# Performance work log

Hardware: AMD Instinct MI355X
Metric: run time of the kernel (lower is better)

Reference implementation:

```python
import jax, jax.numpy as jnp
import numpy as np

B, S, D, H, FF = 2, 2048, 1024, 16, 4096
DK = D // H
LOCAL_WINDOW, STRIDE = 128, 128
NEG = -1000000000.0
EPS = 1e-5


def _layernorm(x, g, b):
    mu = jnp.mean(x, axis=-1, keepdims=True)
    var = jnp.mean(jnp.square(x - mu), axis=-1, keepdims=True)
    return (x - mu) * jax.lax.rsqrt(var + EPS) * g + b


def _strided_mask(seq):
    # allowed(i, j): j <= i and (i-j <= local_window or (i-j) % stride == 0)
    i = jnp.arange(seq)[:, None]
    j = jnp.arange(seq)[None, :]
    d = i - j
    return (d >= 0) & ((d <= LOCAL_WINDOW) | (d % STRIDE == 0))  # [S, S] bool


def setup_inputs() -> dict:
    key = jax.random.key(0)
    ks = jax.random.split(key, 18)
    w = lambda k, shape: jax.random.normal(k, shape, jnp.float32) * 0.02
    return {
        "x": jax.random.normal(ks[0], (B, S, D), jnp.float32),
        "mask": jnp.ones((1, 1, S, S), jnp.int32),
        "Wq": w(ks[1], (D, D)), "bq": jnp.zeros((D,), jnp.float32),
        "Wk": w(ks[2], (D, D)), "bk": jnp.zeros((D,), jnp.float32),
        "Wv": w(ks[3], (D, D)), "bv": jnp.zeros((D,), jnp.float32),
        "Wo": w(ks[4], (D, D)), "bo": jnp.zeros((D,), jnp.float32),
        "W1": w(ks[5], (D, FF)), "bf1": jnp.zeros((FF,), jnp.float32),
        "W2": w(ks[6], (FF, D)), "bf2": jnp.zeros((D,), jnp.float32),
        "g1": jnp.ones((D,), jnp.float32), "bl1": jnp.zeros((D,), jnp.float32),
        "g2": jnp.ones((D,), jnp.float32), "bl2": jnp.zeros((D,), jnp.float32),
    }


def reference(x, mask, Wq, bq, Wk, bk, Wv, bv, Wo, bo,
              W1, bf1, W2, bf2, g1, bl1, g2, bl2):
    b, s, d = x.shape
    sm = _strided_mask(s)[None, None]  # [1,1,S,S]

    # pre-LN self-attention
    n = _layernorm(x, g1, bl1)
    split = lambda t: t.reshape(b, s, H, DK).transpose(0, 2, 1, 3)  # [B,H,S,DK]
    q = split(n @ Wq + bq)
    k = split(n @ Wk + bk)
    v = split(n @ Wv + bv)

    scores = jnp.einsum('bhqd,bhkd->bhqk', q, k) / jnp.sqrt(jnp.float32(DK))
    scores = jnp.where(sm, scores, NEG)          # strided/local mask
    scores = jnp.where(mask == 0, NEG, scores)   # user mask
    attn = jax.nn.softmax(scores, axis=-1)
    o = jnp.einsum('bhqk,bhkd->bhqd', attn, v)
    o = o.transpose(0, 2, 1, 3).reshape(b, s, d) @ Wo + bo
    x = x + o

    # pre-LN FFN (GELU exact, matching torch nn.GELU default)
    n2 = _layernorm(x, g2, bl2)
    ff = jax.nn.gelu(n2 @ W1 + bf1, approximate=False) @ W2 + bf2
    return x + ff
```

## Files before the change

### kernel.cpp

```cpp
#include <hip/hip_runtime.h>
#include <math.h>

typedef unsigned int u32;
typedef unsigned short u16;

#define B_  2
#define S_  2048
#define D_  1024
#define H_  16
#define DK_ 64
#define FF_ 4096
#define NEG_ -1000000000.0f

typedef __attribute__((ext_vector_type(8))) short short8;
typedef __attribute__((ext_vector_type(4))) float floatx4;
typedef __attribute__((ext_vector_type(4))) unsigned short ushort4_t;

__device__ inline u16 f2b(float f) {
    union { float f; u32 u; } v; v.f = f;
    u32 r = (v.u + 0x7fffu + ((v.u >> 16) & 1u)) >> 16;
    return (u16)r;
}
__device__ inline float b2f(u16 b) {
    union { u32 u; float f; } v; v.u = ((u32)b) << 16;
    return v.f;
}

__device__ inline void gl_lds16(const u16* g, u16* l) {
    __builtin_amdgcn_global_load_lds((const __attribute__((address_space(1))) u32*)g,
                                     (__attribute__((address_space(3))) u32*)l, 16, 0, 0);
}

__global__ void tconv4(const float* __restrict__ W0, const float* __restrict__ W1_,
                       const float* __restrict__ W2_, const float* __restrict__ W3,
                       u16* __restrict__ dstBase) {
    __shared__ float tile[32][33];
    int z = blockIdx.z;
    const float* Wm = (z == 0) ? W0 : (z == 1) ? W1_ : (z == 2) ? W2_ : W3;
    u16* Wt = dstBase + (size_t)z * 1024 * 1024;
    const int K = 1024, N = 1024;
    int n0 = blockIdx.x * 32, k0 = blockIdx.y * 32;
    int tx = threadIdx.x & 31, ty = threadIdx.x >> 5;
#pragma unroll
    for (int r = 0; r < 32; r += 8)
        tile[ty + r][tx] = Wm[(size_t)(k0 + ty + r) * N + n0 + tx];
    __syncthreads();
#pragma unroll
    for (int r = 0; r < 32; r += 8)
        Wt[(size_t)(n0 + ty + r) * K + k0 + tx] = f2b(tile[tx][ty + r]);
}

__global__ void tconv(const float* __restrict__ Wm, u16* __restrict__ Wt, int K, int N) {
    __shared__ float tile[32][33];
    int n0 = blockIdx.x * 32, k0 = blockIdx.y * 32;
    int tx = threadIdx.x & 31, ty = threadIdx.x >> 5;
#pragma unroll
    for (int r = 0; r < 32; r += 8)
        tile[ty + r][tx] = Wm[(size_t)(k0 + ty + r) * N + n0 + tx];
    __syncthreads();
#pragma unroll
    for (int r = 0; r < 32; r += 8)
        Wt[(size_t)(n0 + ty + r) * K + k0 + tx] = f2b(tile[tx][ty + r]);
}

__global__ void catbias(const float* __restrict__ bq, const float* __restrict__ bk,
                        const float* __restrict__ bv, float* __restrict__ out) {
    int i = blockIdx.x * 256 + threadIdx.x;
    float v = (i < 1024) ? bq[i] : (i < 2048) ? bk[i - 1024] : bv[i - 2048];
    out[i] = v;
}

__global__ __launch_bounds__(256)
void mask_tiles(const int* __restrict__ mask, int* __restrict__ tflag) {
    int jt = blockIdx.x, it = blockIdx.y;
    const int* base = mask + (size_t)it * 128 * S_ + jt * 128;
    int t = threadIdx.x;
    int ok = 1;
    for (int e = t; e < 128 * 32; e += 256) {
        int r = e >> 5, c4 = e & 31;
        int4 vv = *(const int4*)&base[(size_t)r * S_ + c4 * 4];
        ok &= (vv.x != 0) & (vv.y != 0) & (vv.z != 0) & (vv.w != 0);
    }
    ok = (int)__all(ok);
    __shared__ int red[4];
    if ((t & 63) == 0) red[t >> 6] = ok;
    __syncthreads();
    if (t == 0) tflag[it * 16 + jt] = red[0] & red[1] & red[2] & red[3];
}

__global__ void ln_bf16(const float* __restrict__ x, const float* __restrict__ g,
                        const float* __restrict__ b, u16* __restrict__ out) {
    int row = blockIdx.x;
    int t = threadIdx.x;
    const float* xr = x + (size_t)row * D_;
    __shared__ float red[256];

    float v[4];
    float s = 0.f;
#pragma unroll
    for (int i = 0; i < 4; i++) { v[i] = xr[i * 256 + t]; s += v[i]; }
    red[t] = s; __syncthreads();
    for (int off = 128; off > 0; off >>= 1) {
        if (t < off) red[t] += red[t + off];
        __syncthreads();
    }
    float mu = red[0] * (1.0f / D_);
    __syncthreads();

    float vs = 0.f;
#pragma unroll
    for (int i = 0; i < 4; i++) { float d = v[i] - mu; vs += d * d; }
    red[t] = vs; __syncthreads();
    for (int off = 128; off > 0; off >>= 1) {
        if (t < off) red[t] += red[t + off];
        __syncthreads();
    }
    float rstd = rsqrtf(red[0] * (1.0f / D_) + 1e-5f);

    u16* outr = out + (size_t)row * D_;
#pragma unroll
    for (int i = 0; i < 4; i++) {
        int col = i * 256 + t;
        outr[col] = f2b((v[i] - mu) * rstd * g[col] + b[col]);
    }
}

__global__ __launch_bounds__(256)
void merge_ln(const u16* __restrict__ P, const float* __restrict__ x,
              const float* __restrict__ bo, const float* __restrict__ g,
              const float* __restrict__ bl, float* __restrict__ x1,
              u16* __restrict__ n2) {
    const size_t MN = (size_t)B_ * S_ * D_;
    int row = blockIdx.x, t = threadIdx.x;
    size_t base = (size_t)row * D_;
    __shared__ float red[256];

    float v[4];
    float s = 0.f;
#pragma unroll
    for (int i = 0; i < 4; i++) {
        int col = i * 256 + t;
        float val = x[base + col] + bo[col] + b2f(P[base + col]) + b2f(P[MN + base + col]);
        v[i] = val; s += val;
    }
    red[t] = s; __syncthreads();
    for (int off = 128; off > 0; off >>= 1) {
        if (t < off) red[t] += red[t + off];
        __syncthreads();
    }
    float mu = red[0] * (1.0f / D_);
    __syncthreads();

    float vs = 0.f;
#pragma unroll
    for (int i = 0; i < 4; i++) { float d = v[i] - mu; vs += d * d; }
    red[t] = vs; __syncthreads();
    for (int off = 128; off > 0; off >>= 1) {
        if (t < off) red[t] += red[t + off];
        __syncthreads();
    }
    float rstd = rsqrtf(red[0] * (1.0f / D_) + 1e-5f);

#pragma unroll
    for (int i = 0; i < 4; i++) {
        int col = i * 256 + t;
        x1[base + col] = v[i];
        n2[base + col] = f2b((v[i] - mu) * rstd * g[col] + bl[col]);
    }
}

template <int EPI>
__global__ __launch_bounds__(256, 4)
void gemm_bt(const u16* __restrict__ A, const u16* __restrict__ Bt,
             const float* __restrict__ bias, const float* __restrict__ R,
             void* __restrict__ Cv, int M, int N, int K, int ldA, int ldB) {
    __shared__ u16 As[2][128 * 32];
    __shared__ u16 Bs[2][128 * 32];
    int tid = threadIdx.x;
    int lane = tid & 63, w = tid >> 6;
    int wm = w >> 1, wn = w & 1;
    int m0 = blockIdx.x * 128, n0 = blockIdx.y * 128;
    size_t koff = (size_t)blockIdx.z * K;

    floatx4 acc[4][4];
#pragma unroll
    for (int a = 0; a < 4; a++)
#pragma unroll
        for (int b2 = 0; b2 < 4; b2++) acc[a][b2] = (floatx4){0.f, 0.f, 0.f, 0.f};

    int r4 = lane >> 2;
    int qg = ((lane & 3) ^ ((lane >> 3) & 3)) * 8;
    const u16* Ag0 = A + (size_t)(m0 + w * 16 + r4) * ldA + koff + qg;
    const u16* Bg0 = Bt + (size_t)(n0 + w * 16 + r4) * ldB + koff + qg;
    const int ldsOff = (w * 16) * 32;

    int c = lane & 15, g = lane >> 4;
    int sw = (g ^ ((c >> 1) & 3)) * 8;

    const int nIter = K >> 5;

    gl_lds16(Ag0, &As[0][ldsOff]);
    gl_lds16(Ag0 + (size_t)64 * ldA, &As[0][ldsOff + 64 * 32]);
    gl_lds16(Bg0, &Bs[0][ldsOff]);
    gl_lds16(Bg0 + (size_t)64 * ldB, &Bs[0][ldsOff + 64 * 32]);

    for (int it = 0; it < nIter; it++) {
        __syncthreads();
        int cur = it & 1, nxt = cur ^ 1;
        if (it + 1 < nIter) {
            int kk = (it + 1) << 5;
            gl_lds16(Ag0 + kk, &As[nxt][ldsOff]);
            gl_lds16(Ag0 + kk + (size_t)64 * ldA, &As[nxt][ldsOff + 64 * 32]);
            gl_lds16(Bg0 + kk, &Bs[nxt][ldsOff]);
            gl_lds16(Bg0 + kk + (size_t)64 * ldB, &Bs[nxt][ldsOff + 64 * 32]);
        }
        short8 fa[4], fb[4];
#pragma unroll
        for (int a = 0; a < 4; a++)
            fa[a] = *(const short8*)&As[cur][(wm * 64 + a * 16 + c) * 32 + sw];
#pragma unroll
        for (int b2 = 0; b2 < 4; b2++)
            fb[b2] = *(const short8*)&Bs[cur][(wn * 64 + b2 * 16 + c) * 32 + sw];
#pragma unroll
        for (int a = 0; a < 4; a++)
#pragma unroll
            for (int b2 = 0; b2 < 4; b2++)
                acc[a][b2] = __builtin_amdgcn_mfma_f32_16x16x32_bf16(fa[a], fb[b2], acc[a][b2], 0, 0, 0);
    }

    int mb = m0 + wm * 64, nb = n0 + wn * 64;
#pragma unroll
    for (int a = 0; a < 4; a++) {
#pragma unroll
        for (int b2 = 0; b2 < 4; b2++) {
            int mrow = mb + a * 16 + g * 4;
            int ncol = nb + b2 * 16 + c;
            float bv = (EPI == 3) ? 0.f : bias[ncol];
#pragma unroll
            for (int r = 0; r < 4; r++) {
                int m = mrow + r;
                float vvv = acc[a][b2][r] + bv;
                if (EPI == 0) {
                    int which = ncol >> 10, col = ncol & 1023;
                    if (which == 0) vvv *= 0.125f;
                    int bb = m >> 11, ss = m & 2047, hh = col >> 6, dk = col & 63;
                    ((u16*)Cv)[(size_t)which * ((size_t)B_ * S_ * D_) +
                               ((((size_t)bb * H_ + hh) * S_) + ss) * DK_ + dk] = f2b(vvv);
                } else if (EPI == 1) {
                    ((float*)Cv)[(size_t)m * N + ncol] = vvv + R[(size_t)m * N + ncol];
                } else if (EPI == 2) {
                    float u = 0.79788456080286536f * fmaf(0.044715f * vvv, vvv * vvv, vvv);
                    float th = 1.f - 2.f / (1.f + __expf(2.f * u));
                    ((u16*)Cv)[(size_t)m * N + ncol] = f2b(0.5f * vvv * (1.f + th));
                } else {
                    ((u16*)Cv)[(size_t)blockIdx.z * M * N + (size_t)m * N + ncol] = f2b(vvv);
                }
            }
        }
    }
}

__global__ __launch_bounds__(256)
void ffn2_merge(const u16* __restrict__ P, const float* __restrict__ x1,
                const float* __restrict__ bf2, float* __restrict__ out) {
    const size_t MN = (size_t)B_ * S_ * D_;
    int e = (blockIdx.x * 256 + threadIdx.x) * 4;
    float4 xv = *(const float4*)&x1[e];
    float4 bv = *(const float4*)&bf2[e & 1023];
    float o0 = xv.x + bv.x, o1 = xv.y + bv.y, o2 = xv.z + bv.z, o3 = xv.w + bv.w;
#pragma unroll
    for (int z = 0; z < 4; z++) {
        ushort4_t pv = *(const ushort4_t*)&P[z * MN + e];
        o0 += b2f(pv[0]); o1 += b2f(pv[1]); o2 += b2f(pv[2]); o3 += b2f(pv[3]);
    }
    *(float4*)&out[e] = (float4){o0, o1, o2, o3};
}

#define MAXB_ 14
__global__ __launch_bounds__(256)
void attn4(const u16* __restrict__ q, const u16* __restrict__ k,
           const u16* __restrict__ v, const int* __restrict__ mask,
           const int* __restrict__ tileOK, u16* __restrict__ ob) {
    __shared__ u16 sh[26624];
    u16* Kw = sh;
    u16* Vt = sh + 13824;
    u16* Qs = Vt;

    const int i0 = blockIdx.x * 64;
    const int bh = blockIdx.y;
    const int b  = bh >> 4, h = bh & 15;
    const int t  = threadIdx.x;
    const int lane = t & 63, w = t >> 6;
    const int c = lane & 15, g = lane >> 4;
    const int g4 = g * 4;
    const int qloc16 = w * 16;

    const u16* qg = q + ((size_t)bh * S_ + i0) * DK_;
    const u16* kg = k + (size_t)bh * S_ * DK_;
    const u16* vg = v + (size_t)bh * S_ * DK_;

    const int wlo = (i0 >= 128) ? i0 - 128 : 0;
    const int wn  = i0 + 64 - wlo;
    const int nb  = (i0 >= 256) ? (i0 >> 7) - 1 : 0;
    const int jb0 = i0 & 127;
    const int dd0 = i0 - wlo;

    bool allOK = true;
    {
        const int* rowf = tileOK + (i0 >> 7) * 16;
        int jt0 = wlo >> 7, jt1 = (i0 + 63) >> 7;
        for (int jt = jt0; jt <= jt1; jt++) allOK &= (rowf[jt] != 0);
        for (int m = 0; m < nb; m++) allOK &= (rowf[m] != 0);
    }

    for (int e = t; e < 64 * 8; e += 256) {
        int row = e >> 3, dc = e & 7;
        *(short8*)&Qs[row * 72 + dc * 8] = *(const short8*)(qg + row * 64 + dc * 8);
    }
    for (int e = t; e < wn * 8; e += 256) {
        int row = e >> 3, dc = e & 7;
        *(short8*)&Kw[row * 72 + dc * 8] = *(const short8*)(kg + (size_t)(wlo + row) * 64 + dc * 8);
    }
    __syncthreads();

    float sbr[MAXB_];
    {
        short8 qv0 = *(const short8*)&Qs[(qloc16 + c) * 72 + g * 8];
        short8 qv1 = *(const short8*)&Qs[(qloc16 + c) * 72 + 32 + g * 8];
#pragma unroll
        for (int m = 0; m < MAXB_; m++) {
            sbr[m] = NEG_;
            if (m < nb) {
                int jrow = jb0 + (m << 7) + qloc16 + c;
                short8 kv0 = *(const short8*)(kg + (size_t)jrow * 64 + g * 8);
                short8 kv1 = *(const short8*)(kg + (size_t)jrow * 64 + 32 + g * 8);
                float p = 0.f;
#pragma unroll
                for (int i = 0; i < 8; i++) {
                    p += b2f((u16)qv0[i]) * b2f((u16)kv0[i]);
                    p += b2f((u16)qv1[i]) * b2f((u16)kv1[i]);
                }
                p += __shfl_xor(p, 16);
                p += __shfl_xor(p, 32);
                if (!allOK && mask[(size_t)(i0 + qloc16 + c) * S_ + jrow] == 0) p = NEG_;
                sbr[m] = p;
            }
        }
    }

    floatx4 sc[12];
#pragma unroll
    for (int ct = 0; ct < 12; ct++) sc[ct] = (floatx4){0.f, 0.f, 0.f, 0.f};
    {
        short8 fa0 = *(const short8*)&Qs[(qloc16 + c) * 72 + g * 8];
        short8 fa1 = *(const short8*)&Qs[(qloc16 + c) * 72 + 32 + g * 8];
#pragma unroll
        for (int ct = 0; ct < 12; ct++) {
            short8 fb0 = *(const short8*)&Kw[(ct * 16 + c) * 72 + g * 8];
            short8 fb1 = *(const short8*)&Kw[(ct * 16 + c) * 72 + 32 + g * 8];
            sc[ct] = __builtin_amdgcn_mfma_f32_16x16x32_bf16(fa0, fb0, sc[ct], 0, 0, 0);
            sc[ct] = __builtin_amdgcn_mfma_f32_16x16x32_bf16(fa1, fb1, sc[ct], 0, 0, 0);
        }
    }

#pragma unroll
    for (int ct = 0; ct < 12; ct++) {
        int cidx = ct * 16 + c;
        int j = wlo + cidx;
#pragma unroll
        for (int r = 0; r < 4; r++) {
            int qloc = qloc16 + g4 + r;
            int d = dd0 + qloc - cidx;
            bool ok = (d >= 0) && (d <= 128);
            if (ok && !allOK) ok = (mask[(size_t)(i0 + qloc) * S_ + j] != 0);
            sc[ct][r] = ok ? sc[ct][r] : NEG_;
        }
    }

    float mv[4], inv[4];
#pragma unroll
    for (int r = 0; r < 4; r++) {
        float bs[MAXB_];
#pragma unroll
        for (int m = 0; m < MAXB_; m++)
            bs[m] = (m < nb) ? __shfl(sbr[m], g4 + r, 64) : NEG_;
        float mm = -1e30f;
#pragma unroll
        for (int ct = 0; ct < 12; ct++) mm = fmaxf(mm, sc[ct][r]);
        mm = fmaxf(mm, __shfl_xor(mm, 1));
        mm = fmaxf(mm, __shfl_xor(mm, 2));
        mm = fmaxf(mm, __shfl_xor(mm, 4));
        mm = fmaxf(mm, __shfl_xor(mm, 8));
#pragma unroll
        for (int m = 0; m < MAXB_; m++)
            if (m < nb) mm = fmaxf(mm, bs[m]);
        float sum = 0.f;
#pragma unroll
        for (int ct = 0; ct < 12; ct++) {
            float e = __expf(sc[ct][r] - mm);
            sc[ct][r] = e;
            sum += e;
        }
        sum += __shfl_xor(sum, 1);
        sum += __shfl_xor(sum, 2);
        sum += __shfl_xor(sum, 4);
        sum += __shfl_xor(sum, 8);
#pragma unroll
        for (int m = 0; m < MAXB_; m++)
            if (m < nb) sum += __expf(bs[m] - mm);
        mv[r] = mm;
        inv[r] = 1.f / sum;
    }

    __syncthreads();
    u16* P = Kw;
#pragma unroll
    for (int ct = 0; ct < 12; ct++)
#pragma unroll
        for (int r = 0; r < 4; r++)
            P[(qloc16 + g4 + r) * 200 + ct * 16 + c] = f2b(sc[ct][r]);
#pragma unroll
    for (int dc = 0; dc < 8; dc++) {
        for (int jl = t; jl < 192; jl += 256) {
            short8 val = {0, 0, 0, 0, 0, 0, 0, 0};
            if (jl < wn) val = *(const short8*)(vg + (size_t)(wlo + jl) * 64 + dc * 8);
#pragma unroll
            for (int i = 0; i < 8; i++) Vt[(dc * 8 + i) * 200 + jl] = (u16)val[i];
        }
    }
    __syncthreads();

    floatx4 o[4];
#pragma unroll
    for (int nt = 0; nt < 4; nt++) o[nt] = (floatx4){0.f, 0.f, 0.f, 0.f};
#pragma unroll
    for (int ks = 0; ks < 6; ks++) {
        short8 pa = *(const short8*)&P[(qloc16 + c) * 200 + ks * 32 + g * 8];
#pragma unroll
        for (int nt = 0; nt < 4; nt++) {
            short8 vb = *(const short8*)&Vt[(nt * 16 + c) * 200 + ks * 32 + g * 8];
            o[nt] = __builtin_amdgcn_mfma_f32_16x16x32_bf16(pa, vb, o[nt], 0, 0, 0);
        }
    }

#pragma unroll
    for (int m = 0; m < MAXB_; m++) {
        if (m < nb) {
            int vbase = jb0 + (m << 7) + qloc16 + g4;
            u16 vv[4][4];
#pragma unroll
            for (int r = 0; r < 4; r++)
#pragma unroll
                for (int nt = 0; nt < 4; nt++)
                    vv[r][nt] = vg[(size_t)(vbase + r) * 64 + nt * 16 + c];
#pragma unroll
            for (int r = 0; r < 4; r++) {
                float bs = __shfl(sbr[m], g4 + r, 64);
                float pb = __expf(bs - mv[r]);
#pragma unroll
                for (int nt = 0; nt < 4; nt++)
                    o[nt][r] += pb * b2f(vv[r][nt]);
            }
        }
    }

#pragma unroll
    for (int nt = 0; nt < 4; nt++) {
#pragma unroll
        for (int r = 0; r < 4; r++) {
            int qi = i0 + qloc16 + g4 + r;
            ob[((size_t)b * S_ + qi) * D_ + h * 64 + nt * 16 + c] = f2b(o[nt][r] * inv[r]);
        }
    }
}

extern "C" void kernel_launch(void* const* d_in, const int* in_sizes, int n_in,
                              void* d_out, int out_size, void* d_ws, size_t ws_size,
                              hipStream_t stream) {
    const float* x    = (const float*)d_in[0];
    const int*   mask = (const int*)  d_in[1];
    const float* Wq   = (const float*)d_in[2];
    const float* bq   = (const float*)d_in[3];
    const float* Wk   = (const float*)d_in[4];
    const float* bk   = (const float*)d_in[5];
    const float* Wv   = (const float*)d_in[6];
    const float* bv   = (const float*)d_in[7];
    const float* Wo   = (const float*)d_in[8];
    const float* bo   = (const float*)d_in[9];
    const float* W1   = (const float*)d_in[10];
    const float* bf1  = (const float*)d_in[11];
    const float* W2   = (const float*)d_in[12];
    const float* bf2  = (const float*)d_in[13];
    const float* g1   = (const float*)d_in[14];
    const float* bl1  = (const float*)d_in[15];
    const float* g2   = (const float*)d_in[16];
    const float* bl2  = (const float*)d_in[17];

    char* wsb = (char*)d_ws;
    const size_t MB = 1024 * 1024;
    u16*   WtQKV  = (u16*)(wsb + 0);
    u16*   WtO    = (u16*)(wsb + 6 * MB);
    u16*   Wt1    = (u16*)(wsb + 8 * MB);
    u16*   Wt2    = (u16*)(wsb + 16 * MB);
    u16*   n1b    = (u16*)(wsb + 24 * MB);
    u16*   qkv    = (u16*)(wsb + 32 * MB);
    u16*   obb    = (u16*)(wsb + 56 * MB);
    float* x1     = (float*)(wsb + 32 * MB);
    u16*   ff1b   = (u16*)(wsb + 48 * MB);
    u16*   Ppart  = (u16*)(wsb + 82 * MB);
    u16*   PpartO = (u16*)(wsb + 82 * MB);
    float* bcat   = (float*)(wsb + 114 * MB);
    int*   tflag  = (int*)(wsb + 115 * MB);
    u16*   n2b    = n1b;

    const int M = B_ * S_;
    const size_t SZ = (size_t)B_ * S_ * D_;

    mask_tiles<<<dim3(16, 16), 256, 0, stream>>>(mask, tflag);
    tconv4<<<dim3(32, 32, 4), 256, 0, stream>>>(Wq, Wk, Wv, Wo, WtQKV);
    tconv<<<dim3(128, 32), 256, 0, stream>>>(W1, Wt1, 1024, 4096);
    tconv<<<dim3(32, 128), 256, 0, stream>>>(W2, Wt2, 4096, 1024);
    catbias<<<12, 256, 0, stream>>>(bq, bk, bv, bcat);

    ln_bf16<<<M, 256, 0, stream>>>(x, g1, bl1, n1b);

    gemm_bt<0><<<dim3(32, 24), 256, 0, stream>>>(n1b, WtQKV, bcat, nullptr, qkv,
                                                 M, 3072, 1024, 1024, 1024);

    attn4<<<dim3(32, 32), 256, 0, stream>>>(qkv, qkv + SZ, qkv + 2 * SZ, mask, tflag, obb);

    gemm_bt<3><<<dim3(32, 8, 2), 256, 0, stream>>>(obb, WtO, nullptr, nullptr, PpartO,
                                                   M, 1024, 512, 1024, 1024);
    merge_ln<<<M, 256, 0, stream>>>(PpartO, x, bo, g2, bl2, x1, n2b);

    gemm_bt<2><<<dim3(32, 32), 256, 0, stream>>>(n2b, Wt1, bf1, nullptr, ff1b,
                                                 M, 4096, 1024, 1024, 1024);

    gemm_bt<3><<<dim3(32, 8, 4), 256, 0, stream>>>(ff1b, Wt2, nullptr, nullptr, Ppart,
                                                   M, 1024, 1024, 4096, 4096);
    ffn2_merge<<<(int)(SZ / 1024), 256, 0, stream>>>(Ppart, x1, bf2, (float*)d_out);
}
```

Before: 382.2 us.

## Pre-transpose V in a separate kernel and read V^T directly from global in attention

Adds a vtrans kernel that writes V transposed per head into a spare workspace buffer (reusing the n1b region). The attention kernel then loads its PV MFMA B-operands straight from this global V^T instead of staging and transposing V through shared memory. This drops the in-kernel LDS transpose loop and one barrier, and shrinks the shared-memory footprint, which may allow more blocks per CU. In exchange it adds an extra launch plus a full read and write of V, and the MFMA operands now come from global/L2 with a strided row layout rather than from LDS.

```diff
diff --git a/kernel.cpp b/kernel.cpp
--- a/kernel.cpp
+++ b/kernel.cpp
@@ -61,6 +61,22 @@
 #pragma unroll
     for (int r = 0; r < 32; r += 8)
         Wt[(size_t)(n0 + ty + r) * K + k0 + tx] = f2b(tile[tx][ty + r]);
+}
+
+__global__ __launch_bounds__(256)
+void vtrans(const u16* __restrict__ v, u16* __restrict__ vt) {
+    __shared__ u16 t[32][33];
+    int bh = blockIdx.z, s0 = blockIdx.x * 32, d0 = blockIdx.y * 32;
+    const u16* vp = v + (size_t)bh * S_ * DK_;
+    u16* op = vt + (size_t)bh * DK_ * S_;
+    int tx = threadIdx.x & 31, ty = threadIdx.x >> 5;
+#pragma unroll
+    for (int r = 0; r < 32; r += 8)
+        t[ty + r][tx] = vp[(size_t)(s0 + ty + r) * DK_ + d0 + tx];
+    __syncthreads();
+#pragma unroll
+    for (int r = 0; r < 32; r += 8)
+        op[(size_t)(d0 + ty + r) * S_ + s0 + tx] = t[tx][ty + r];
 }
 
 __global__ void catbias(const float* __restrict__ bq, const float* __restrict__ bk,
@@ -279,12 +295,12 @@
 #define MAXB_ 14
 __global__ __launch_bounds__(256)
 void attn4(const u16* __restrict__ q, const u16* __restrict__ k,
-           const u16* __restrict__ v, const int* __restrict__ mask,
-           const int* __restrict__ tileOK, u16* __restrict__ ob) {
-    __shared__ u16 sh[26624];
+           const u16* __restrict__ v, const u16* __restrict__ vtg,
+           const int* __restrict__ mask, const int* __restrict__ tileOK,
+           u16* __restrict__ ob) {
+    __shared__ u16 sh[18432];
     u16* Kw = sh;
-    u16* Vt = sh + 13824;
-    u16* Qs = Vt;
+    u16* Qs = sh + 13824;
 
     const int i0 = blockIdx.x * 64;
     const int bh = blockIdx.y;
@@ -298,6 +314,7 @@
     const u16* qg = q + ((size_t)bh * S_ + i0) * DK_;
     const u16* kg = k + (size_t)bh * S_ * DK_;
     const u16* vg = v + (size_t)bh * S_ * DK_;
+    const u16* vtb = vtg + (size_t)bh * DK_ * S_;
 
     const int wlo = (i0 >= 128) ? i0 - 128 : 0;
     const int wn  = i0 + 64 - wlo;
@@ -419,16 +436,6 @@
 #pragma unroll
         for (int r = 0; r < 4; r++)
             P[(qloc16 + g4 + r) * 200 + ct * 16 + c] = f2b(sc[ct][r]);
-#pragma unroll
-    for (int dc = 0; dc < 8; dc++) {
-        for (int jl = t; jl < 192; jl += 256) {
-            short8 val = {0, 0, 0, 0, 0, 0, 0, 0};
-            if (jl < wn) val = *(const short8*)(vg + (size_t)(wlo + jl) * 64 + dc * 8);
-#pragma unroll
-            for (int i = 0; i < 8; i++) Vt[(dc * 8 + i) * 200 + jl] = (u16)val[i];
-        }
-    }
-    __syncthreads();
 
     floatx4 o[4];
 #pragma unroll
@@ -438,7 +445,7 @@
         short8 pa = *(const short8*)&P[(qloc16 + c) * 200 + ks * 32 + g * 8];
 #pragma unroll
         for (int nt = 0; nt < 4; nt++) {
-            short8 vb = *(const short8*)&Vt[(nt * 16 + c) * 200 + ks * 32 + g * 8];
+            short8 vb = *(const short8*)&vtb[(size_t)(nt * 16 + c) * S_ + wlo + ks * 32 + g * 8];
             o[nt] = __builtin_amdgcn_mfma_f32_16x16x32_bf16(pa, vb, o[nt], 0, 0, 0);
         }
     }
@@ -511,6 +518,7 @@
     u16*   PpartO = (u16*)(wsb + 82 * MB);
     float* bcat   = (float*)(wsb + 114 * MB);
     int*   tflag  = (int*)(wsb + 115 * MB);
+    u16*   vt     = n1b;
     u16*   n2b    = n1b;
 
     const int M = B_ * S_;
@@ -527,7 +535,9 @@
     gemm_bt<0><<<dim3(32, 24), 256, 0, stream>>>(n1b, WtQKV, bcat, nullptr, qkv,
                                                  M, 3072, 1024, 1024, 1024);
 
-    attn4<<<dim3(32, 32), 256, 0, stream>>>(qkv, qkv + SZ, qkv + 2 * SZ, mask, tflag, obb);
+    vtrans<<<dim3(64, 2, 32), 256, 0, stream>>>(qkv + 2 * SZ, vt);
+
+    attn4<<<dim3(32, 32), 256, 0, stream>>>(qkv, qkv + SZ, qkv + 2 * SZ, vt, mask, tflag, obb);
 
     gemm_bt<3><<<dim3(32, 8, 2), 256, 0, stream>>>(obb, WtO, nullptr, nullptr, PpartO,
                                                    M, 1024, 512, 1024, 1024);
```

Result: slower. 400.7 us (+4.8%).

## Split V transpose into two halves to shrink attention LDS and reorder grid

Applied to the files above, without the earlier changes.

The attention kernel now stages the transposed V window in two 96-column halves, reusing one smaller LDS buffer instead of a full 192-column one. This cuts shared memory per block from about 53KB to about 39KB so more blocks can be resident per CU. The grid is also reordered so the head index is blockIdx.x and query tiles run in reverse order, so the longer late tiles are scheduled first. The cost is an extra pair of barriers and a second V staging pass whenever the window is wider than 96.

```diff
diff --git a/kernel.cpp b/kernel.cpp
--- a/kernel.cpp
+++ b/kernel.cpp
@@ -281,13 +281,13 @@
 void attn4(const u16* __restrict__ q, const u16* __restrict__ k,
            const u16* __restrict__ v, const int* __restrict__ mask,
            const int* __restrict__ tileOK, u16* __restrict__ ob) {
-    __shared__ u16 sh[26624];
+    __shared__ u16 sh[19456];
     u16* Kw = sh;
-    u16* Vt = sh + 13824;
-    u16* Qs = Vt;
-
-    const int i0 = blockIdx.x * 64;
-    const int bh = blockIdx.y;
+    u16* Qs = sh + 13824;
+    u16* Vh = sh + 12800;
+
+    const int bh = blockIdx.x;
+    const int i0 = (31 - blockIdx.y) * 64;
     const int b  = bh >> 4, h = bh & 15;
     const int t  = threadIdx.x;
     const int lane = t & 63, w = t >> 6;
@@ -419,27 +419,48 @@
 #pragma unroll
         for (int r = 0; r < 4; r++)
             P[(qloc16 + g4 + r) * 200 + ct * 16 + c] = f2b(sc[ct][r]);
-#pragma unroll
-    for (int dc = 0; dc < 8; dc++) {
-        for (int jl = t; jl < 192; jl += 256) {
+
+    for (int e = t; e < 768; e += 256) {
+        int dc = e / 96, jl = e - dc * 96;
+        short8 val = {0, 0, 0, 0, 0, 0, 0, 0};
+        if (jl < wn) val = *(const short8*)(vg + (size_t)(wlo + jl) * 64 + dc * 8);
+#pragma unroll
+        for (int i = 0; i < 8; i++) Vh[(dc * 8 + i) * 104 + jl] = (u16)val[i];
+    }
+    __syncthreads();
+
+    floatx4 o[4];
+#pragma unroll
+    for (int nt = 0; nt < 4; nt++) o[nt] = (floatx4){0.f, 0.f, 0.f, 0.f};
+#pragma unroll
+    for (int ks = 0; ks < 3; ks++) {
+        short8 pa = *(const short8*)&P[(qloc16 + c) * 200 + ks * 32 + g * 8];
+#pragma unroll
+        for (int nt = 0; nt < 4; nt++) {
+            short8 vb = *(const short8*)&Vh[(nt * 16 + c) * 104 + ks * 32 + g * 8];
+            o[nt] = __builtin_amdgcn_mfma_f32_16x16x32_bf16(pa, vb, o[nt], 0, 0, 0);
+        }
+    }
+
+    if (wn > 96) {
+        __syncthreads();
+        for (int e = t; e < 768; e += 256) {
+            int dc = e / 96, jl = e - dc * 96;
+            int j2 = 96 + jl;
             short8 val = {0, 0, 0, 0, 0, 0, 0, 0};
-            if (jl < wn) val = *(const short8*)(vg + (size_t)(wlo + jl) * 64 + dc * 8);
-#pragma unroll
-            for (int i = 0; i < 8; i++) Vt[(dc * 8 + i) * 200 + jl] = (u16)val[i];
-        }
-    }
-    __syncthreads();
-
-    floatx4 o[4];
-#pragma unroll
-    for (int nt = 0; nt < 4; nt++) o[nt] = (floatx4){0.f, 0.f, 0.f, 0.f};
-#pragma unroll
-    for (int ks = 0; ks < 6; ks++) {
-        short8 pa = *(const short8*)&P[(qloc16 + c) * 200 + ks * 32 + g * 8];
-#pragma unroll
-        for (int nt = 0; nt < 4; nt++) {
-            short8 vb = *(const short8*)&Vt[(nt * 16 + c) * 200 + ks * 32 + g * 8];
-            o[nt] = __builtin_amdgcn_mfma_f32_16x16x32_bf16(pa, vb, o[nt], 0, 0, 0);
+            if (j2 < wn) val = *(const short8*)(vg + (size_t)(wlo + j2) * 64 + dc * 8);
+#pragma unroll
+            for (int i = 0; i < 8; i++) Vh[(dc * 8 + i) * 104 + jl] = (u16)val[i];
+        }
+        __syncthreads();
+#pragma unroll
+        for (int ks = 0; ks < 3; ks++) {
+            short8 pa = *(const short8*)&P[(qloc16 + c) * 200 + 96 + ks * 32 + g * 8];
+#pragma unroll
+            for (int nt = 0; nt < 4; nt++) {
+                short8 vb = *(const short8*)&Vh[(nt * 16 + c) * 104 + ks * 32 + g * 8];
+                o[nt] = __builtin_amdgcn_mfma_f32_16x16x32_bf16(pa, vb, o[nt], 0, 0, 0);
+            }
         }
     }
 
```

New measurement: 371.5 us. 1.03x faster.
